# Kernel tuning notes

Measured on AMD Instinct MI355X. Metric: run time of the kernel, lower is better.

## Reference

```python
import jax, jax.numpy as jnp
import numpy as np

EPS = 1e-12

def squash(s):
    # standard capsule squash: ||s||^2/(1+||s||^2) * s/||s||
    n2 = jnp.sum(s * s, axis=-1, keepdims=True)
    return n2 / (1.0 + n2) * s / jnp.sqrt(n2 + EPS)

def setup_inputs() -> dict:
    key = jax.random.key(0)
    k1, k2 = jax.random.split(key)
    B, O, I, DOUT, DIN = 64, 32, 2048, 16, 16
    u = jax.random.normal(k1, (B, I, DIN), dtype=jnp.float32)
    # TruncatedNormal(stddev=0.1) init for W
    W = 0.1 * jax.random.truncated_normal(k2, -2.0, 2.0, (1, O, I, DOUT, DIN), dtype=jnp.float32)
    bias = jnp.full((1, O, DOUT), 0.1, dtype=jnp.float32)
    return {"u": u, "W": W, "bias": bias}

def reference(u, W, bias):
    routing_iterations = 3
    O = W.shape[1]
    # u: [B, I, DIN], W: [1, O, I, DOUT, DIN]
    u_norm = jnp.linalg.norm(u, axis=-1)                     # [B, I]
    # u_hat[b,o,i,d] = sum_k W[0,o,i,d,k] * u[b,i,k]  (batched matmul instead of tile+mul+sum)
    u_hat = jnp.einsum('oidk,bik->boid', W[0], u)            # [B, O, I, DOUT]
    u_hat_norm = jnp.linalg.norm(u_hat, axis=-1, keepdims=True)   # [B, O, I, 1]
    new_u_hat_norm = jnp.minimum(u_hat_norm, u_norm[:, None, :, None])
    u_hat = u_hat / (u_hat_norm + EPS) * new_u_hat_norm

    B = u.shape[0]
    b_ij = jnp.zeros((B, O, u.shape[1], 1), dtype=u.dtype)
    t_const = jnp.float32(np.log(0.9 * (O - 1)) - np.log(1.0 - 0.9))
    v_j = None
    c_ij = None
    for r in range(routing_iterations):
        c_ij = jax.nn.softmax(b_ij, axis=1)                  # softmax over out capsules
        s_j = jnp.sum(c_ij * u_hat, axis=2) + bias           # [B, O, DOUT]
        v_j = squash(s_j)
        if r < routing_iterations - 1:
            # gamma-routing agreement: distance between prediction and output
            d = jnp.linalg.norm(v_j[:, :, None, :] - u_hat, axis=-1, keepdims=True)  # [B,O,I,1]
            d_o = jnp.mean(d)
            d_p = d_o * 0.5
            t = t_const / (d_p - d_o + 1e-12)
            b_ij = t * d
    return (v_j, c_ij)
```

## Files before the change

### kernel.cpp

```cpp
#include <hip/hip_runtime.h>
#include <hip/hip_bf16.h>
#include <hip/hip_fp16.h>
#include <math.h>

#define BB 64
#define OO 32
#define II 2048
#define DD 16
#define CAPS_EPS 1e-12f
#define T_CONST 5.6312118f

#define TIS 16
#define SLEN 16
#define NSTRIP 128

#define OFF_DSUM  0ULL
#define OFF_V     16ULL
#define OFF_UNORM 32784ULL
#define OFF_UBF   163856ULL
#define OFF_Y     1212432ULL
#define OFF_DD    34766864ULL
#define OFF_TMAX  36864016ULL
#define OFF_TDEN  36995088ULL
#define OFF_PART  37126160ULL
#define OFF_VT    39223312ULL

typedef __attribute__((ext_vector_type(8))) short bf16x8;
typedef __attribute__((ext_vector_type(4))) float f32x4;

union AU { bf16x8 v; unsigned short h[8]; uint4 u4; };
union YU { __half h[4]; uint2 u2; };
union YL { uint4 u4[2]; __half h[16]; };
union PS { __half h[16]; uint4 u4[2]; };
union P4 { __half h[4]; uint2 u2; };

__device__ __forceinline__ unsigned short f2bf(float x) {
    __hip_bfloat16 h = __float2bfloat16(x);
    unsigned short s; __builtin_memcpy(&s, &h, 2); return s;
}

__global__ __launch_bounds__(256) void uprep_kernel(
    const float* __restrict__ u, float* __restrict__ ws)
{
    const int gid = blockIdx.x * 256 + threadIdx.x;
    if (gid < 2) ws[OFF_DSUM + gid] = 0.f;
    const int i = gid >> 6, b = gid & 63;

    const float4* up = reinterpret_cast<const float4*>(u + ((size_t)b * II + i) * DD);
    float4 t0 = up[0], t1 = up[1], t2 = up[2], t3 = up[3];
    float un2 = t0.x*t0.x + t0.y*t0.y + t0.z*t0.z + t0.w*t0.w
              + t1.x*t1.x + t1.y*t1.y + t1.z*t1.z + t1.w*t1.w
              + t2.x*t2.x + t2.y*t2.y + t2.z*t2.z + t2.w*t2.w
              + t3.x*t3.x + t3.y*t3.y + t3.z*t3.z + t3.w*t3.w;
    ws[OFF_UNORM + (size_t)i * 64 + b] = __builtin_amdgcn_sqrtf(un2);

    AU a0, a1;
    a0.h[0]=f2bf(t0.x); a0.h[1]=f2bf(t0.y); a0.h[2]=f2bf(t0.z); a0.h[3]=f2bf(t0.w);
    a0.h[4]=f2bf(t1.x); a0.h[5]=f2bf(t1.y); a0.h[6]=f2bf(t1.z); a0.h[7]=f2bf(t1.w);
    a1.h[0]=f2bf(t2.x); a1.h[1]=f2bf(t2.y); a1.h[2]=f2bf(t2.z); a1.h[3]=f2bf(t2.w);
    a1.h[4]=f2bf(t3.x); a1.h[5]=f2bf(t3.y); a1.h[6]=f2bf(t3.z); a1.h[7]=f2bf(t3.w);
    unsigned short* ubf = (unsigned short*)(ws + OFF_UBF);
    uint4* dst = reinterpret_cast<uint4*>(ubf + ((size_t)i * 64 + b) * 16);
    dst[0] = a0.u4; dst[1] = a1.u4;
}

__global__ __launch_bounds__(256) void s0w_kernel(
    const float* __restrict__ W, float* __restrict__ ws)
{
    const int strip = blockIdx.x;
    const int og   = blockIdx.y;
    const int wave = threadIdx.x >> 6;
    const int lane = threadIdx.x & 63;
    const int o    = og * 4 + wave;
    const int q    = lane >> 4;
    const int n    = lane & 15;

    const unsigned short* ubf = (const unsigned short*)(ws + OFF_UBF);
    const float* unorm = ws + OFF_UNORM;
    __half* Y = (__half*)(ws + OFF_Y);
    __half* part_h = (__half*)(ws + OFF_PART);

    f32x4 s_acc[4];
    #pragma unroll
    for (int g = 0; g < 4; ++g) s_acc[g] = (f32x4){0.f, 0.f, 0.f, 0.f};

    for (int ii = 0; ii < TIS; ++ii) {
        const int i = strip * TIS + ii;

        AU au; au.u4 = make_uint4(0, 0, 0, 0);
        if (q < 2) {
            const float* wp = W + (((size_t)o * II + i) * 16 + n) * 16 + q * 8;
            float4 w0 = *(const float4*)(wp);
            float4 w1 = *(const float4*)(wp + 4);
            au.h[0]=f2bf(w0.x); au.h[1]=f2bf(w0.y); au.h[2]=f2bf(w0.z); au.h[3]=f2bf(w0.w);
            au.h[4]=f2bf(w1.x); au.h[5]=f2bf(w1.y); au.h[6]=f2bf(w1.z); au.h[7]=f2bf(w1.w);
        }

        f32x4 d4[4];
        #pragma unroll
        for (int g = 0; g < 4; ++g) {
            AU bu;
            bu.u4 = *reinterpret_cast<const uint4*>(
                ubf + ((size_t)i * 64 + g * 16 + n) * 16 + (q & 1) * 8);
            d4[g] = __builtin_amdgcn_mfma_f32_16x16x32_bf16(
                au.v, bu.v, (f32x4){0.f, 0.f, 0.f, 0.f}, 0, 0, 0);
        }

        #pragma unroll
        for (int g = 0; g < 4; ++g) {
            float n2 = d4[g][0]*d4[g][0] + d4[g][1]*d4[g][1]
                     + d4[g][2]*d4[g][2] + d4[g][3]*d4[g][3];
            n2 += __shfl_xor(n2, 16);
            n2 += __shfl_xor(n2, 32);
            const float rsq  = __builtin_amdgcn_rsqf(n2 + CAPS_EPS);
            const float rawn = n2 * rsq;
            const float un = unorm[(size_t)i * 64 + g * 16 + n];
            const float scale = fminf(rawn, un) * rsq;

            YU yu;
            yu.h[0] = __float2half(scale * d4[g][0]);
            yu.h[1] = __float2half(scale * d4[g][1]);
            yu.h[2] = __float2half(scale * d4[g][2]);
            yu.h[3] = __float2half(scale * d4[g][3]);
            *reinterpret_cast<uint2*>(
                Y + (((size_t)i * OO + o) * 64 + g * 16 + n) * 16 + q * 4) = yu.u2;

            const float cs = 0.03125f * scale;
            s_acc[g][0] += cs * d4[g][0];
            s_acc[g][1] += cs * d4[g][1];
            s_acc[g][2] += cs * d4[g][2];
            s_acc[g][3] += cs * d4[g][3];
        }
    }

    #pragma unroll
    for (int g = 0; g < 4; ++g) {
        P4 pu;
        pu.h[0] = __float2half(s_acc[g][0]);
        pu.h[1] = __float2half(s_acc[g][1]);
        pu.h[2] = __float2half(s_acc[g][2]);
        pu.h[3] = __float2half(s_acc[g][3]);
        *reinterpret_cast<uint2*>(
            part_h + (((size_t)strip * OO + o) * 64 + g * 16 + n) * 16 + q * 4) = pu.u2;
    }
}

template<int FINAL>
__global__ __launch_bounds__(256) void finv_kernel(
    float* __restrict__ ws, const float* __restrict__ bias,
    float* __restrict__ out)
{
    const int tid = blockIdx.x * 256 + threadIdx.x;
    const int b = tid >> 9, o = (tid >> 4) & 31, d = tid & 15;
    const __half* part_h = (const __half*)(ws + OFF_PART);
    const size_t base = ((size_t)o * 64 + b) * 16 + d;
    float s = 0.f;
    #pragma unroll 4
    for (int st = 0; st < NSTRIP; ++st)
        s += __half2float(part_h[(size_t)st * (OO * 64 * 16) + base]);
    s += bias[tid & 511];
    float n2 = s * s;
    #pragma unroll
    for (int off = 1; off < 16; off <<= 1) n2 += __shfl_xor(n2, off);
    const float val = s * n2 * __builtin_amdgcn_rcpf(1.f + n2)
                        * __builtin_amdgcn_rsqf(n2 + CAPS_EPS);
    if (FINAL) out[tid] = val;
    else       ws[OFF_VT + base] = val;
}

template<int SLOT>
__global__ __launch_bounds__(256) void dpass_kernel(float* __restrict__ ws)
{
    const int strip = blockIdx.x;
    const int og    = blockIdx.y;
    const int wave  = threadIdx.x >> 6;
    const int b     = threadIdx.x & 63;
    const int o     = og * 4 + wave;

    const __half* Y  = (const __half*)(ws + OFF_Y);
    const float* vt  = ws + OFF_VT;
    __half* dws = (__half*)(ws + OFF_DD);

    float v[16];
    {
        const float4* vp = reinterpret_cast<const float4*>(
            vt + ((size_t)o * 64 + b) * 16);
        float4 a = vp[0], c = vp[1], e = vp[2], f = vp[3];
        v[0]=a.x; v[1]=a.y; v[2]=a.z; v[3]=a.w;
        v[4]=c.x; v[5]=c.y; v[6]=c.z; v[7]=c.w;
        v[8]=e.x; v[9]=e.y; v[10]=e.z; v[11]=e.w;
        v[12]=f.x; v[13]=f.y; v[14]=f.z; v[15]=f.w;
    }
    float vn2 = 0.f;
    #pragma unroll
    for (int k = 0; k < 16; ++k) vn2 += v[k] * v[k];

    float acc = 0.f;
    #pragma unroll 4
    for (int s = 0; s < SLEN; ++s) {
        const int i = strip * SLEN + s;
        const uint4* yp = reinterpret_cast<const uint4*>(
            Y + (((size_t)i * OO + o) * 64 + b) * 16);
        YL yl;
        yl.u4[0] = yp[0];
        yl.u4[1] = yp[1];
        float dot = 0.f, yn2 = 0.f;
        #pragma unroll
        for (int k = 0; k < 16; ++k) {
            const float y = __half2float(yl.h[k]);
            dot += v[k] * y;
            yn2 += y * y;
        }
        const float dd2 = fmaxf(vn2 - 2.f * dot + yn2, 0.f);
        const __half dh = __float2half(__builtin_amdgcn_sqrtf(dd2));
        dws[((size_t)i * OO + o) * 64 + b] = dh;
        acc += __half2float(dh);
    }

    #pragma unroll
    for (int off = 32; off > 0; off >>= 1) acc += __shfl_down(acc, off);
    __shared__ float red[4];
    if ((threadIdx.x & 63) == 0) red[wave] = acc;
    __syncthreads();
    if (threadIdx.x == 0)
        atomicAdd(&ws[OFF_DSUM + SLOT], red[0] + red[1] + red[2] + red[3]);
}

template<int SLOT>
__global__ __launch_bounds__(256) void csoft_kernel(float* __restrict__ ws)
{
    const int gid = blockIdx.x * 256 + threadIdx.x;
    const int i = gid >> 6, b = gid & 63;

    const __half* dws = (const __half*)(ws + OFF_DD);
    const float dsum = ws[OFF_DSUM + SLOT];
    const float tval = T_CONST * __builtin_amdgcn_rcpf(
        -0.5f * dsum * (1.0f / 4194304.0f) + 1e-12f);

    float dv[OO];
    #pragma unroll
    for (int o = 0; o < OO; ++o)
        dv[o] = tval * __half2float(dws[((size_t)i * OO + o) * 64 + b]);
    float m = -1e30f;
    #pragma unroll
    for (int o = 0; o < OO; ++o) m = fmaxf(m, dv[o]);
    float den = 0.f;
    #pragma unroll
    for (int o = 0; o < OO; ++o) den += __expf(dv[o] - m);
    ws[OFF_TMAX + (size_t)i * 64 + b] = m;
    ws[OFF_TDEN + (size_t)i * 64 + b] = den;
}

template<int SLOT>
__global__ __launch_bounds__(256) void spass_kernel(float* __restrict__ ws)
{
    const int strip = blockIdx.x;
    const int og    = blockIdx.y;
    const int wave  = threadIdx.x >> 6;
    const int b     = threadIdx.x & 63;
    const int o     = og * 4 + wave;

    const __half* Y = (const __half*)(ws + OFF_Y);
    const __half* dws = (const __half*)(ws + OFF_DD);
    const float* tmax = ws + OFF_TMAX;
    const float* tden = ws + OFF_TDEN;
    __half* part_h = (__half*)(ws + OFF_PART);

    const float dsum = ws[OFF_DSUM + SLOT];
    const float tval = T_CONST * __builtin_amdgcn_rcpf(
        -0.5f * dsum * (1.0f / 4194304.0f) + 1e-12f);

    float acc[16];
    #pragma unroll
    for (int k = 0; k < 16; ++k) acc[k] = 0.f;

    #pragma unroll 4
    for (int s = 0; s < SLEN; ++s) {
        const int i = strip * SLEN + s;
        const uint4* yp = reinterpret_cast<const uint4*>(
            Y + (((size_t)i * OO + o) * 64 + b) * 16);
        YL yl;
        yl.u4[0] = yp[0];
        yl.u4[1] = yp[1];
        const float d  = __half2float(dws[((size_t)i * OO + o) * 64 + b]);
        const float m  = tmax[(size_t)i * 64 + b];
        const float dn = tden[(size_t)i * 64 + b];
        const float p = __expf(tval * d - m) * __builtin_amdgcn_rcpf(dn);
        #pragma unroll
        for (int k = 0; k < 16; ++k)
            acc[k] += p * __half2float(yl.h[k]);
    }

    PS su;
    #pragma unroll
    for (int k = 0; k < 16; ++k) su.h[k] = __float2half(acc[k]);
    uint4* pp = reinterpret_cast<uint4*>(
        part_h + (((size_t)strip * OO + o) * 64 + b) * 16);
    pp[0] = su.u4[0];
    pp[1] = su.u4[1];
}

__global__ __launch_bounds__(256) void transpose_kernel(
    const float* __restrict__ ws, float* __restrict__ dst)
{
    __shared__ float tile[32][65];
    const __half* dws = (const __half*)(ws + OFF_DD);
    const float* tmax = ws + OFF_TMAX;
    const float* tden = ws + OFF_TDEN;
    const float dsum = ws[OFF_DSUM + 1];
    const float tval = T_CONST * __builtin_amdgcn_rcpf(
        -0.5f * dsum * (1.0f / 4194304.0f) + 1e-12f);

    const int o  = blockIdx.y;
    const int i0 = blockIdx.x * 32;
    #pragma unroll
    for (int k = 0; k < 8; ++k) {
        const int lin = k * 256 + threadIdx.x;
        const int r = lin >> 6, b = lin & 63;
        const int i = i0 + r;
        const float d = __half2float(dws[((size_t)i * OO + o) * 64 + b]);
        tile[r][b] = __expf(tval * d - tmax[(size_t)i * 64 + b])
                   * __builtin_amdgcn_rcpf(tden[(size_t)i * 64 + b]);
    }
    __syncthreads();
    #pragma unroll
    for (int k = 0; k < 8; ++k) {
        const int lin = k * 256 + threadIdx.x;
        const int b = lin >> 5, r = lin & 31;
        dst[((size_t)b * OO + o) * II + i0 + r] = tile[r][b];
    }
}

extern "C" void kernel_launch(void* const* d_in, const int* in_sizes, int n_in,
                              void* d_out, int out_size, void* d_ws, size_t ws_size,
                              hipStream_t stream) {
    const float* u    = (const float*)d_in[0];
    const float* W    = (const float*)d_in[1];
    const float* bias = (const float*)d_in[2];
    float* out = (float*)d_out;
    float* ws  = (float*)d_ws;

    float* cout = out + (size_t)BB * OO * DD;

    dim3 blk(256);
    dim3 grid_s(NSTRIP, 8);

    uprep_kernel<<<512, blk, 0, stream>>>(u, ws);
    s0w_kernel<<<grid_s, blk, 0, stream>>>(W, ws);
    finv_kernel<0><<<128, blk, 0, stream>>>(ws, bias, out);
    dpass_kernel<0><<<grid_s, blk, 0, stream>>>(ws);
    csoft_kernel<0><<<512, blk, 0, stream>>>(ws);
    spass_kernel<0><<<grid_s, blk, 0, stream>>>(ws);
    finv_kernel<0><<<128, blk, 0, stream>>>(ws, bias, out);
    dpass_kernel<1><<<grid_s, blk, 0, stream>>>(ws);
    csoft_kernel<1><<<512, blk, 0, stream>>>(ws);
    spass_kernel<1><<<grid_s, blk, 0, stream>>>(ws);
    finv_kernel<1><<<128, blk, 0, stream>>>(ws, bias, out);
    transpose_kernel<<<dim3(64, 32), blk, 0, stream>>>(ws, cout);
}
```

Measured before the change: 321.8 us.

## Split strip reduction into two-stage kernels and double s0w strip count

```diff
diff --git a/kernel.cpp b/kernel.cpp
--- a/kernel.cpp
+++ b/kernel.cpp
@@ -10,7 +10,8 @@
 #define CAPS_EPS 1e-12f
 #define T_CONST 5.6312118f
 
-#define TIS 16
+#define TIS 8
+#define NSTRIP_W 256
 #define SLEN 16
 #define NSTRIP 128
 
@@ -23,7 +24,8 @@
 #define OFF_TMAX  36864016ULL
 #define OFF_TDEN  36995088ULL
 #define OFF_PART  37126160ULL
-#define OFF_VT    39223312ULL
+#define OFF_VT    41320464ULL
+#define OFF_P2    41353232ULL
 
 typedef __attribute__((ext_vector_type(8))) short bf16x8;
 typedef __attribute__((ext_vector_type(4))) float f32x4;
@@ -145,27 +147,40 @@
     }
 }
 
+template<int NS>
+__global__ __launch_bounds__(256) void fpart_kernel(float* __restrict__ ws)
+{
+    const int tid = blockIdx.x * 256 + threadIdx.x;
+    const int g = tid >> 15;
+    const int x = tid & 32767;
+    const __half* part_h = (const __half*)(ws + OFF_PART);
+    constexpr int NSG = NS / 8;
+    float s = 0.f;
+    #pragma unroll
+    for (int k = 0; k < NSG; ++k)
+        s += __half2float(part_h[(size_t)(g * NSG + k) * 32768 + x]);
+    ws[OFF_P2 + (size_t)g * 32768 + x] = s;
+}
+
 template<int FINAL>
-__global__ __launch_bounds__(256) void finv_kernel(
+__global__ __launch_bounds__(256) void fsquash_kernel(
     float* __restrict__ ws, const float* __restrict__ bias,
     float* __restrict__ out)
 {
     const int tid = blockIdx.x * 256 + threadIdx.x;
     const int b = tid >> 9, o = (tid >> 4) & 31, d = tid & 15;
-    const __half* part_h = (const __half*)(ws + OFF_PART);
-    const size_t base = ((size_t)o * 64 + b) * 16 + d;
-    float s = 0.f;
-    #pragma unroll 4
-    for (int st = 0; st < NSTRIP; ++st)
-        s += __half2float(part_h[(size_t)st * (OO * 64 * 16) + base]);
-    s += bias[tid & 511];
+    const size_t px = ((size_t)o * 64 + b) * 16 + d;
+    float s = bias[tid & 511];
+    #pragma unroll
+    for (int g = 0; g < 8; ++g)
+        s += ws[OFF_P2 + (size_t)g * 32768 + px];
     float n2 = s * s;
     #pragma unroll
     for (int off = 1; off < 16; off <<= 1) n2 += __shfl_xor(n2, off);
     const float val = s * n2 * __builtin_amdgcn_rcpf(1.f + n2)
                         * __builtin_amdgcn_rsqf(n2 + CAPS_EPS);
     if (FINAL) out[tid] = val;
-    else       ws[OFF_VT + base] = val;
+    else       ws[OFF_VT + px] = val;
 }
 
 template<int SLOT>
@@ -343,18 +358,22 @@
     float* cout = out + (size_t)BB * OO * DD;
 
     dim3 blk(256);
+    dim3 grid_w(NSTRIP_W, 8);
     dim3 grid_s(NSTRIP, 8);
 
     uprep_kernel<<<512, blk, 0, stream>>>(u, ws);
-    s0w_kernel<<<grid_s, blk, 0, stream>>>(W, ws);
-    finv_kernel<0><<<128, blk, 0, stream>>>(ws, bias, out);
+    s0w_kernel<<<grid_w, blk, 0, stream>>>(W, ws);
+    fpart_kernel<NSTRIP_W><<<1024, blk, 0, stream>>>(ws);
+    fsquash_kernel<0><<<128, blk, 0, stream>>>(ws, bias, out);
     dpass_kernel<0><<<grid_s, blk, 0, stream>>>(ws);
     csoft_kernel<0><<<512, blk, 0, stream>>>(ws);
     spass_kernel<0><<<grid_s, blk, 0, stream>>>(ws);
-    finv_kernel<0><<<128, blk, 0, stream>>>(ws, bias, out);
+    fpart_kernel<NSTRIP><<<1024, blk, 0, stream>>>(ws);
+    fsquash_kernel<0><<<128, blk, 0, stream>>>(ws, bias, out);
     dpass_kernel<1><<<grid_s, blk, 0, stream>>>(ws);
     csoft_kernel<1><<<512, blk, 0, stream>>>(ws);
     spass_kernel<1><<<grid_s, blk, 0, stream>>>(ws);
-    finv_kernel<1><<<128, blk, 0, stream>>>(ws, bias, out);
+    fpart_kernel<NSTRIP><<<1024, blk, 0, stream>>>(ws);
+    fsquash_kernel<1><<<128, blk, 0, stream>>>(ws, bias, out);
     transpose_kernel<<<dim3(64, 32), blk, 0, stream>>>(ws, cout);
 }
```

Measured after the change: 291.5 us (median of 2 runs). 9.4% less time.
